# Kernel tuning notes

Hardware: AMD Instinct MI355X
Metric: run time of the kernel (lower is better)

Reference implementation:

```python
import jax, jax.numpy as jnp
import numpy as np

B, L, HID, D, H, HKV, EPS, THETA = 1, 2048, 2048, 128, 32, 4, 1e-6, 1000000.0
GROUPS = H // HKV  # 8


def setup_inputs() -> dict:
    key = jax.random.key(0)
    ks = jax.random.split(key, 6)
    x = jax.random.normal(ks[0], (B, L, HID), dtype=jnp.float32)
    wq = jax.random.normal(ks[1], (H * D, HID), dtype=jnp.float32) * 0.02
    wk = jax.random.normal(ks[2], (HKV * D, HID), dtype=jnp.float32) * 0.02
    wv = jax.random.normal(ks[3], (HKV * D, HID), dtype=jnp.float32) * 0.02
    wo = jax.random.normal(ks[4], (HID, H * D), dtype=jnp.float32) * 0.02
    q_norm_w = jnp.ones((D,), dtype=jnp.float32)
    k_norm_w = jnp.ones((D,), dtype=jnp.float32)
    # RoPE tables: inv_freq over half dims, emb = concat(freqs, freqs)
    inv_freq = 1.0 / (THETA ** (jnp.arange(0, D, 2, dtype=jnp.float32) / D))
    pos = jnp.arange(L, dtype=jnp.float32)
    freqs = pos[:, None] * inv_freq[None, :]        # [L, D/2]
    emb = jnp.concatenate([freqs, freqs], axis=-1)  # [L, D]
    cos = jnp.cos(emb)[None]                        # [1, L, D]
    sin = jnp.sin(emb)[None]
    return {"x": x, "wq": wq, "wk": wk, "wv": wv, "wo": wo,
            "q_norm_w": q_norm_w, "k_norm_w": k_norm_w, "cos": cos, "sin": sin}


def _rmsnorm(t, w):
    var = jnp.mean(t * t, axis=-1, keepdims=True)
    return t * jax.lax.rsqrt(var + EPS) * w


def _rotate_half(t):
    t1, t2 = jnp.split(t, 2, axis=-1)
    return jnp.concatenate([-t2, t1], axis=-1)


def reference(x, wq, wk, wv, wo, q_norm_w, k_norm_w, cos, sin):
    b, l, _ = x.shape
    # projections -> [B, heads, L, D]
    q = _rmsnorm((x @ wq.T).reshape(b, l, H, D), q_norm_w).swapaxes(1, 2)
    k = _rmsnorm((x @ wk.T).reshape(b, l, HKV, D), k_norm_w).swapaxes(1, 2)
    v = (x @ wv.T).reshape(b, l, HKV, D).swapaxes(1, 2)
    # RoPE (cos/sin broadcast over head dim)
    c, s = cos[:, None], sin[:, None]
    q = c * q + s * _rotate_half(q)
    k = c * k + s * _rotate_half(k)
    # GQA: repeat kv heads across groups
    k = jnp.repeat(k, GROUPS, axis=1)
    v = jnp.repeat(v, GROUPS, axis=1)
    # causal SDPA
    scores = jnp.einsum("bhqd,bhkd->bhqk", q, k) / np.sqrt(D).astype(np.float32)
    causal = jnp.tril(jnp.ones((l, l), dtype=bool))
    scores = jnp.where(causal, scores, jnp.finfo(scores.dtype).min)
    attn = jax.nn.softmax(scores, axis=-1)
    out = jnp.einsum("bhqk,bhkd->bhqd", attn, v)
    out = out.swapaxes(1, 2).reshape(b, l, H * D)
    return out @ wo.T
```

## Files before the change

### kernel.cpp

```cpp
#include <hip/hip_runtime.h>

typedef unsigned short u16;
typedef short bh8 __attribute__((ext_vector_type(8)));
typedef short bh4 __attribute__((ext_vector_type(4)));
typedef float f4 __attribute__((ext_vector_type(4)));
typedef u16 u16x4 __attribute__((ext_vector_type(4)));

__device__ __forceinline__ u16 f2bf(float f) {
  union { float f; unsigned u; } v; v.f = f;
  unsigned u = v.u;
  return (u16)((u + 0x7fffu + ((u >> 16) & 1u)) >> 16);
}
__device__ __forceinline__ float bf2f(u16 h) {
  union { unsigned u; float f; } v; v.u = ((unsigned)h) << 16;
  return v.f;
}
__device__ __forceinline__ float fast_exp2(float x) {
#if __has_builtin(__builtin_amdgcn_exp2f)
  return __builtin_amdgcn_exp2f(x);
#else
  float r; asm("v_exp_f32 %0, %1" : "=v"(r) : "v"(x)); return r;
#endif
}
__device__ __forceinline__ unsigned cvt_pk_bf16(float lo, float hi) {
  unsigned r;
  asm("v_cvt_pk_bf16_f32 %0, %1, %2" : "=v"(r) : "v"(lo), "v"(hi));
  return r;
}
__device__ __forceinline__ void gll16(const void* src, void* dst) {
  __builtin_amdgcn_global_load_lds((const __attribute__((address_space(1))) void*)src,
                                   (__attribute__((address_space(3))) void*)dst,
                                   16, 0, 0);
}

__global__ __launch_bounds__(256) void k_cvt_all(const float* __restrict__ x,
                                                 const float* __restrict__ wq,
                                                 const float* __restrict__ wk,
                                                 const float* __restrict__ wv,
                                                 const float* __restrict__ wo,
                                                 u16* __restrict__ dst) {
  const size_t n = 5767168;
  for (size_t idx = (size_t)blockIdx.x * 256 + threadIdx.x; idx < n; idx += 4096ull * 256) {
    const float* src; size_t off;
    if (idx < 1048576)       { src = x;  off = idx; }
    else if (idx < 3145728)  { src = wq; off = idx - 1048576; }
    else if (idx < 3407872)  { src = wk; off = idx - 3145728; }
    else if (idx < 3670016)  { src = wv; off = idx - 3407872; }
    else                     { src = wo; off = idx - 3670016; }
    f4 v = *(const f4*)(src + off * 4);
    u16x4 o;
    o.x = f2bf(v[0]); o.y = f2bf(v[1]); o.z = f2bf(v[2]); o.w = f2bf(v[3]);
    *(u16x4*)(dst + idx * 4) = o;
  }
}

template<int K, bool OUTF32, int NFR, bool FUSED>
__global__ __launch_bounds__(256) void k_gemm(const u16* __restrict__ A,
                                              const u16* __restrict__ B1,
                                              const u16* __restrict__ B2,
                                              void* __restrict__ C1,
                                              void* __restrict__ C2,
                                              int N1, int N2, int NB1, int npx) {
  constexpr int BN = NFR * 32;
  constexpr int nk = K / 32;
  __shared__ u16 As[3][128 * 32];
  __shared__ u16 Bs[3][BN * 32];
  const int t = threadIdx.x;
  const int lane = t & 63;
  const int w = t >> 6, wm = w >> 1, wn = w & 1;
  const int g = lane >> 4, r16 = lane & 15;
  const int bb = blockIdx.x;
  const int gl = (bb & 7) * npx + (bb >> 3);
  const int bm = gl & 15;
  int bn = gl >> 4;

  const u16* B; void* C; int N;
  if (!FUSED || bn < NB1) { B = B1; C = C1; N = N1; }
  else { bn -= NB1; B = B2; C = C2; N = N2; }
  B += (size_t)bn * BN * K;

  f4 acc[4][NFR] = {};

  const int rA0 = t >> 2, cA0 = (t & 3) * 8;
  const u16* a0 = A + (size_t)(bm * 128 + rA0) * K + cA0;
  const u16* a1 = a0 + (size_t)64 * K;
  const u16* b0 = B + (size_t)rA0 * K + cA0;

  auto STAGE = [&](int kk, int bi) {
    gll16(a0 + kk * 32, As[bi] + t * 8);
    gll16(a1 + kk * 32, As[bi] + (t + 256) * 8);
    gll16(b0 + kk * 32, Bs[bi] + t * 8);
    if constexpr (BN == 128) gll16(b0 + (size_t)64 * K + kk * 32, Bs[bi] + (t + 256) * 8);
  };
  auto COMP = [&](int bi) {
    bh8 af[4], bfr[NFR];
#pragma unroll
    for (int m = 0; m < 4; ++m)
      af[m] = *(const bh8*)&As[bi][(wm * 64 + m * 16 + r16) * 32 + g * 8];
#pragma unroll
    for (int n = 0; n < NFR; ++n)
      bfr[n] = *(const bh8*)&Bs[bi][(wn * 16 * NFR + n * 16 + r16) * 32 + g * 8];
    __builtin_amdgcn_s_setprio(1);
#pragma unroll
    for (int m = 0; m < 4; ++m)
#pragma unroll
      for (int n = 0; n < NFR; ++n)
        acc[m][n] = __builtin_amdgcn_mfma_f32_16x16x32_bf16(af[m], bfr[n], acc[m][n], 0, 0, 0);
    __builtin_amdgcn_s_setprio(0);
  };

  STAGE(0, 0);
  STAGE(1, 1);

  int bi = 0;
  for (int k = 0; k < nk - 2; ++k) {
    int st = bi + 2; if (st >= 3) st -= 3;
    STAGE(k + 2, st);
    if constexpr (BN == 128) asm volatile("s_waitcnt vmcnt(8)" ::: "memory");
    else                     asm volatile("s_waitcnt vmcnt(6)" ::: "memory");
    __builtin_amdgcn_s_barrier();
    __builtin_amdgcn_sched_barrier(0);
    COMP(bi);
    asm volatile("s_waitcnt lgkmcnt(0)" ::: "memory");
    __builtin_amdgcn_s_barrier();
    bi = (bi + 1 == 3) ? 0 : bi + 1;
  }
  if constexpr (BN == 128) asm volatile("s_waitcnt vmcnt(4)" ::: "memory");
  else                     asm volatile("s_waitcnt vmcnt(3)" ::: "memory");
  __builtin_amdgcn_s_barrier();
  __builtin_amdgcn_sched_barrier(0);
  COMP(bi);
  asm volatile("s_waitcnt lgkmcnt(0)" ::: "memory");
  __builtin_amdgcn_s_barrier();
  bi = (bi + 1 == 3) ? 0 : bi + 1;
  asm volatile("s_waitcnt vmcnt(0)" ::: "memory");
  __builtin_amdgcn_s_barrier();
  __builtin_amdgcn_sched_barrier(0);
  COMP(bi);

#pragma unroll
  for (int m = 0; m < 4; ++m) {
    const int row0 = bm * 128 + wm * 64 + m * 16 + g * 4;
#pragma unroll
    for (int n = 0; n < NFR; ++n) {
      const int col = bn * BN + wn * 16 * NFR + n * 16 + r16;
#pragma unroll
      for (int r = 0; r < 4; ++r) {
        if constexpr (OUTF32)
          ((float*)C)[(size_t)(row0 + r) * N + col] = acc[m][n][r];
        else
          ((u16*)C)[(size_t)(row0 + r) * N + col] = f2bf(acc[m][n][r]);
      }
    }
  }
}

__global__ __launch_bounds__(256) void k_normrope(u16* __restrict__ qbuf,
                                                  u16* __restrict__ kvbuf,
                                                  const float* __restrict__ qw,
                                                  const float* __restrict__ kw,
                                                  const float* __restrict__ cosb,
                                                  const float* __restrict__ sinb) {
  const float CSC = 1.4426950408889634f * 0.088388347648318447f;
  const int t = threadIdx.x, lane = t & 63, w = t >> 6;
  const int rid = blockIdx.x * 4 + w;
  u16* base; const float* nw; int seq; float sc;
  if (rid < 2048 * 32) {
    seq = rid >> 5;
    base = qbuf + (size_t)seq * 4096 + (size_t)(rid & 31) * 128;
    nw = qw; sc = CSC;
  } else {
    const int r2 = rid - 2048 * 32;
    seq = r2 >> 2;
    base = kvbuf + (size_t)seq * 1024 + (size_t)(r2 & 3) * 128;
    nw = kw; sc = 1.0f;
  }
  float a = bf2f(base[lane]);
  float b = bf2f(base[lane + 64]);
  float ss = a * a + b * b;
#pragma unroll
  for (int off = 32; off >= 1; off >>= 1) ss += __shfl_xor(ss, off);
  const float rs = rsqrtf(ss * (1.0f / 128.0f) + 1e-6f);
  const float na = a * rs * nw[lane];
  const float nb = b * rs * nw[lane + 64];
  const float c1 = cosb[seq * 128 + lane],      s1 = sinb[seq * 128 + lane];
  const float c2 = cosb[seq * 128 + lane + 64], s2 = sinb[seq * 128 + lane + 64];
  base[lane]      = f2bf(sc * (c1 * na - s1 * nb));
  base[lane + 64] = f2bf(sc * (c2 * nb + s2 * na));
}

__global__ __launch_bounds__(256) void k_transpose_v(const u16* __restrict__ kv,
                                                     u16* __restrict__ vt) {
  __shared__ u16 tile[32][33];
  const int t = threadIdx.x;
  const int bl = blockIdx.x, bh = blockIdx.y;
  const int row = t >> 3, c4 = (t & 7) * 4;
  const u16* src = kv + (size_t)(bl * 32 + row) * 1024 + 512 + bh * 32 + c4;
  u16x4 v = *(const u16x4*)src;
  tile[row][c4 + 0] = v.x; tile[row][c4 + 1] = v.y;
  tile[row][c4 + 2] = v.z; tile[row][c4 + 3] = v.w;
  __syncthreads();
  u16x4 o;
  o.x = tile[c4 + 0][row]; o.y = tile[c4 + 1][row];
  o.z = tile[c4 + 2][row]; o.w = tile[c4 + 3][row];
  const int pcol = ((c4 >> 2) & 3) * 8 + (c4 >> 4) * 4;
  *(u16x4*)&vt[(size_t)(bh * 32 + row) * 2048 + bl * 32 + pcol] = o;
}

__global__ __launch_bounds__(256, 3) void k_attn(const u16* __restrict__ Q,
                                                 const u16* __restrict__ Kb,
                                                 const u16* __restrict__ Vt,
                                                 u16* __restrict__ O) {
  __shared__ u16 Ks[2][64 * 128];
  __shared__ u16 Vs[128 * 64];
  const int t = threadIdx.x, lane = t & 63, w = t >> 6;
  const int g = lane >> 4, r16 = lane & 15;
  const int b = blockIdx.x;
  const int i = b & 31;
  const int qt = 31 - (b >> 5);
  const int h = ((i >> 1) & 3) * 8 + ((i & 1) << 2) + (i >> 3);
  const int kvh = h >> 3;
  const int qw0 = qt * 64 + w * 16;
  const int qg  = qw0 + r16;

  bh8 qf[4];
#pragma unroll
  for (int kc = 0; kc < 4; ++kc)
    qf[kc] = *(const bh8*)(Q + (size_t)qg * 4096 + h * 128 + (kc * 4 + g) * 8);

  const int niter = qt + 1;

  f4 acc_o[8] = {};
  f4 acc_l = {};
  float mrun = -3.0e38f;

  bh8 ones;
#pragma unroll
  for (int z = 0; z < 8; ++z) ones[z] = (short)0x3F80;

#pragma unroll
  for (int i2 = 0; i2 < 4; ++i2) {
    const int s = t + 256 * i2, row = s >> 4, sl = s & 15;
    gll16(Kb + (size_t)row * 1024 + kvh * 128 + ((sl ^ (row & 15)) * 8), Ks[0] + s * 8);
  }
  __syncthreads();

  int cur = 0;
  for (int kt = 0; kt < niter; ++kt) {
#pragma unroll
    for (int i2 = 0; i2 < 4; ++i2) {
      const int s = t + 256 * i2, row = s >> 3, sl = s & 7;
      gll16(Vt + (size_t)(kvh * 128 + row) * 2048 + kt * 64 + ((sl ^ (row & 7)) * 8),
            Vs + s * 8);
    }
    if (kt + 1 < niter) {
      const int nt = kt + 1;
#pragma unroll
      for (int i2 = 0; i2 < 4; ++i2) {
        const int s = t + 256 * i2, row = s >> 4, sl = s & 15;
        gll16(Kb + (size_t)(nt * 64 + row) * 1024 + kvh * 128 + ((sl ^ (row & 15)) * 8),
              Ks[cur ^ 1] + s * 8);
      }
    }

    f4 st[4] = {};
    __builtin_amdgcn_s_setprio(1);
#pragma unroll
    for (int kf = 0; kf < 4; ++kf) {
      const int krow = kf * 16 + r16;
#pragma unroll
      for (int kc = 0; kc < 4; ++kc) {
        bh8 kfr = *(const bh8*)&Ks[cur][krow * 128 + (((kc * 4 + g) ^ (krow & 15)) * 8)];
        st[kf] = __builtin_amdgcn_mfma_f32_16x16x32_bf16(kfr, qf[kc], st[kf], 0, 0, 0);
      }
    }
    __builtin_amdgcn_s_setprio(0);

    if (kt == qt) {
      const int kb = kt * 64 + g * 4;
#pragma unroll
      for (int kf = 0; kf < 4; ++kf)
#pragma unroll
        for (int r = 0; r < 4; ++r)
          if (kb + kf * 16 + r > qg) st[kf][r] = -3.0e38f;
    }

    f4 m4;
#pragma unroll
    for (int r = 0; r < 4; ++r)
      m4[r] = fmaxf(fmaxf(st[0][r], st[1][r]), fmaxf(st[2][r], st[3][r]));
    float tmax = fmaxf(fmaxf(m4[0], m4[1]), fmaxf(m4[2], m4[3]));
    tmax = fmaxf(tmax, __shfl_xor(tmax, 16));
    tmax = fmaxf(tmax, __shfl_xor(tmax, 32));

    if (!__all(tmax <= mrun + 8.0f)) {
      const float mnew = fmaxf(mrun, tmax);
      const float alpha = fast_exp2(mrun - mnew);
      mrun = mnew;
      acc_l *= alpha;
#pragma unroll
      for (int d = 0; d < 8; ++d) acc_o[d] *= alpha;
    }

    union { bh8 v[2]; unsigned wrd[8]; } pu;
#pragma unroll
    for (int j = 0; j < 8; ++j) {
      const int i0 = 2 * j, i1 = 2 * j + 1;
      float p0 = fast_exp2(st[i0 >> 2][i0 & 3] - mrun);
      float p1 = fast_exp2(st[i1 >> 2][i1 & 3] - mrun);
      pu.wrd[j] = cvt_pk_bf16(p0, p1);
    }

    __syncthreads();

    __builtin_amdgcn_s_setprio(1);
#pragma unroll
    for (int c = 0; c < 2; ++c)
      acc_l = __builtin_amdgcn_mfma_f32_16x16x32_bf16(ones, pu.v[c], acc_l, 0, 0, 0);
#pragma unroll
    for (int dcol = 0; dcol < 8; ++dcol) {
      const int vrow = dcol * 16 + r16;
#pragma unroll
      for (int c = 0; c < 2; ++c) {
        const int slot = c * 4 + g;
        bh8 vfr = *(const bh8*)&Vs[vrow * 64 + ((slot ^ (vrow & 7)) * 8)];
        acc_o[dcol] = __builtin_amdgcn_mfma_f32_16x16x32_bf16(vfr, pu.v[c], acc_o[dcol], 0, 0, 0);
      }
    }
    __builtin_amdgcn_s_setprio(0);

    __syncthreads();
    cur ^= 1;
  }

  const float inv = 1.0f / acc_l[0];
#pragma unroll
  for (int dcol = 0; dcol < 8; ++dcol) {
    union { u16x4 v; unsigned wrd[2]; } o;
    o.wrd[0] = cvt_pk_bf16(acc_o[dcol][0] * inv, acc_o[dcol][1] * inv);
    o.wrd[1] = cvt_pk_bf16(acc_o[dcol][2] * inv, acc_o[dcol][3] * inv);
    *(u16x4*)&O[(size_t)qg * 4096 + h * 128 + dcol * 16 + g * 4] = o.v;
  }
}

extern "C" void kernel_launch(void* const* d_in, const int* in_sizes, int n_in,
                              void* d_out, int out_size, void* d_ws, size_t ws_size,
                              hipStream_t stream) {
  (void)in_sizes; (void)n_in; (void)out_size; (void)ws_size;
  const float* x    = (const float*)d_in[0];
  const float* wq   = (const float*)d_in[1];
  const float* wk   = (const float*)d_in[2];
  const float* wv   = (const float*)d_in[3];
  const float* wo   = (const float*)d_in[4];
  const float* qw   = (const float*)d_in[5];
  const float* kw   = (const float*)d_in[6];
  const float* cosb = (const float*)d_in[7];
  const float* sinb = (const float*)d_in[8];

  u16* xb   = (u16*)d_ws;
  u16* wqb  = xb  + (size_t)2048 * 2048;
  u16* wkvb = wqb + (size_t)4096 * 2048;
  u16* wob  = wkvb + (size_t)1024 * 2048;
  u16* qbuf = wob + (size_t)2048 * 4096;
  u16* kvb  = qbuf + (size_t)2048 * 4096;
  u16* vt   = kvb + (size_t)2048 * 1024;
  u16* aout = vt  + (size_t)512 * 2048;

  k_cvt_all<<<dim3(4096), 256, 0, stream>>>(x, wq, wk, wv, wo, xb);

  k_gemm<2048, false, 4, true><<<dim3(640), 256, 0, stream>>>(
      xb, wqb, wkvb, qbuf, kvb, 4096, 1024, 32, 80);

  k_normrope<<<dim3((2048 * 36) / 4), 256, 0, stream>>>(qbuf, kvb, qw, kw, cosb, sinb);

  k_transpose_v<<<dim3(64, 16), 256, 0, stream>>>(kvb, vt);

  k_attn<<<dim3(1024), 256, 0, stream>>>(qbuf, kvb, vt, aout);

  k_gemm<4096, true, 2, false><<<dim3(512), 256, 0, stream>>>(
      aout, wob, nullptr, d_out, nullptr, 2048, 0, 0, 64);
}
```

Baseline: 208.3 us.

## Fuse V transpose into QKV GEMM epilogue and deepen K tile for output GEMM

The QKV GEMM now writes V blocks directly in the transposed, permuted layout the attention kernel expects, so the separate transpose kernel and its launch are removed. The shared-memory layout becomes k-group-major so tiles can be staged with a parameterised BK. The output projection GEMM uses BK=64, which halves its k-iterations and barriers but doubles its LDS footprint. This risks layout mismatches in the fused V writes and lower occupancy in the output GEMM.

```diff
diff --git a/kernel.cpp b/kernel.cpp
--- a/kernel.cpp
+++ b/kernel.cpp
@@ -54,17 +54,24 @@
   }
 }
 
-template<int K, bool OUTF32, int NFR, bool FUSED>
+template<int K, bool OUTF32, int NFR, bool FUSED, int BK>
 __global__ __launch_bounds__(256) void k_gemm(const u16* __restrict__ A,
                                               const u16* __restrict__ B1,
                                               const u16* __restrict__ B2,
                                               void* __restrict__ C1,
                                               void* __restrict__ C2,
+                                              u16* __restrict__ Cv,
                                               int N1, int N2, int NB1, int npx) {
   constexpr int BN = NFR * 32;
-  constexpr int nk = K / 32;
-  __shared__ u16 As[3][128 * 32];
-  __shared__ u16 Bs[3][BN * 32];
+  constexpr int nk = K / BK;
+  constexpr int ASZ = 128 * BK;
+  constexpr int BSZ = BN * BK;
+  constexpr int LA = ASZ / 2048;
+  constexpr int LB = BSZ / 2048;
+  constexpr int LPS = LA + LB;
+  constexpr int LOGBN = (BN == 128) ? 7 : 6;
+  __shared__ u16 As[3][ASZ];
+  __shared__ u16 Bs[3][BSZ];
   const int t = threadIdx.x;
   const int lane = t & 63;
   const int w = t >> 6, wm = w >> 1, wn = w & 1;
@@ -74,39 +81,47 @@
   const int bm = gl & 15;
   int bn = gl >> 4;
 
-  const u16* B; void* C; int N;
+  const u16* B; void* C; int N; bool vpath = false;
   if (!FUSED || bn < NB1) { B = B1; C = C1; N = N1; }
-  else { bn -= NB1; B = B2; C = C2; N = N2; }
+  else { bn -= NB1; B = B2; C = C2; N = N2; vpath = (bn >= 4); }
   B += (size_t)bn * BN * K;
+  const u16* Ab = A + (size_t)bm * 128 * K;
 
   f4 acc[4][NFR] = {};
 
-  const int rA0 = t >> 2, cA0 = (t & 3) * 8;
-  const u16* a0 = A + (size_t)(bm * 128 + rA0) * K + cA0;
-  const u16* a1 = a0 + (size_t)64 * K;
-  const u16* b0 = B + (size_t)rA0 * K + cA0;
-
   auto STAGE = [&](int kk, int bi) {
-    gll16(a0 + kk * 32, As[bi] + t * 8);
-    gll16(a1 + kk * 32, As[bi] + (t + 256) * 8);
-    gll16(b0 + kk * 32, Bs[bi] + t * 8);
-    if constexpr (BN == 128) gll16(b0 + (size_t)64 * K + kk * 32, Bs[bi] + (t + 256) * 8);
+    const int k0 = kk * BK;
+#pragma unroll
+    for (int i2 = 0; i2 < LA; ++i2) {
+      const int s = t + 256 * i2;
+      const int g2 = s >> 7, row = s & 127;
+      gll16(Ab + (size_t)row * K + k0 + g2 * 8, As[bi] + s * 8);
+    }
+#pragma unroll
+    for (int i2 = 0; i2 < LB; ++i2) {
+      const int s = t + 256 * i2;
+      const int g2 = s >> LOGBN, col = s & (BN - 1);
+      gll16(B + (size_t)col * K + k0 + g2 * 8, Bs[bi] + s * 8);
+    }
   };
   auto COMP = [&](int bi) {
-    bh8 af[4], bfr[NFR];
-#pragma unroll
-    for (int m = 0; m < 4; ++m)
-      af[m] = *(const bh8*)&As[bi][(wm * 64 + m * 16 + r16) * 32 + g * 8];
-#pragma unroll
-    for (int n = 0; n < NFR; ++n)
-      bfr[n] = *(const bh8*)&Bs[bi][(wn * 16 * NFR + n * 16 + r16) * 32 + g * 8];
-    __builtin_amdgcn_s_setprio(1);
-#pragma unroll
-    for (int m = 0; m < 4; ++m)
+#pragma unroll
+    for (int kk = 0; kk < BK / 32; ++kk) {
+      bh8 af[4], bfr[NFR];
+#pragma unroll
+      for (int m = 0; m < 4; ++m)
+        af[m] = *(const bh8*)&As[bi][((kk * 4 + g) * 128 + (wm * 64 + m * 16 + r16)) * 8];
 #pragma unroll
       for (int n = 0; n < NFR; ++n)
-        acc[m][n] = __builtin_amdgcn_mfma_f32_16x16x32_bf16(af[m], bfr[n], acc[m][n], 0, 0, 0);
-    __builtin_amdgcn_s_setprio(0);
+        bfr[n] = *(const bh8*)&Bs[bi][((kk * 4 + g) * BN + (wn * 16 * NFR + n * 16 + r16)) * 8];
+      __builtin_amdgcn_s_setprio(1);
+#pragma unroll
+      for (int m = 0; m < 4; ++m)
+#pragma unroll
+        for (int n = 0; n < NFR; ++n)
+          acc[m][n] = __builtin_amdgcn_mfma_f32_16x16x32_bf16(af[m], bfr[n], acc[m][n], 0, 0, 0);
+      __builtin_amdgcn_s_setprio(0);
+    }
   };
 
   STAGE(0, 0);
@@ -116,8 +131,8 @@
   for (int k = 0; k < nk - 2; ++k) {
     int st = bi + 2; if (st >= 3) st -= 3;
     STAGE(k + 2, st);
-    if constexpr (BN == 128) asm volatile("s_waitcnt vmcnt(8)" ::: "memory");
-    else                     asm volatile("s_waitcnt vmcnt(6)" ::: "memory");
+    if constexpr (LPS == 4) asm volatile("s_waitcnt vmcnt(8)" ::: "memory");
+    else                    asm volatile("s_waitcnt vmcnt(12)" ::: "memory");
     __builtin_amdgcn_s_barrier();
     __builtin_amdgcn_sched_barrier(0);
     COMP(bi);
@@ -125,8 +140,8 @@
     __builtin_amdgcn_s_barrier();
     bi = (bi + 1 == 3) ? 0 : bi + 1;
   }
-  if constexpr (BN == 128) asm volatile("s_waitcnt vmcnt(4)" ::: "memory");
-  else                     asm volatile("s_waitcnt vmcnt(3)" ::: "memory");
+  if constexpr (LPS == 4) asm volatile("s_waitcnt vmcnt(4)" ::: "memory");
+  else                    asm volatile("s_waitcnt vmcnt(6)" ::: "memory");
   __builtin_amdgcn_s_barrier();
   __builtin_amdgcn_sched_barrier(0);
   COMP(bi);
@@ -137,6 +152,24 @@
   __builtin_amdgcn_s_barrier();
   __builtin_amdgcn_sched_barrier(0);
   COMP(bi);
+
+  if constexpr (FUSED) {
+    if (vpath) {
+#pragma unroll
+      for (int m = 0; m < 4; ++m) {
+        const int lp = bm * 128 + wm * 64 + (m >> 1) * 32 + g * 8 + (m & 1) * 4;
+#pragma unroll
+        for (int n = 0; n < NFR; ++n) {
+          const int col = bn * BN + wn * 16 * NFR + n * 16 + r16;
+          union { u16x4 v; unsigned wrd[2]; } o;
+          o.wrd[0] = cvt_pk_bf16(acc[m][n][0], acc[m][n][1]);
+          o.wrd[1] = cvt_pk_bf16(acc[m][n][2], acc[m][n][3]);
+          *(u16x4*)&Cv[(size_t)(col - 512) * 2048 + lp] = o.v;
+        }
+      }
+      return;
+    }
+  }
 
 #pragma unroll
   for (int m = 0; m < 4; ++m) {
@@ -189,24 +222,6 @@
   base[lane + 64] = f2bf(sc * (c2 * nb + s2 * na));
 }
 
-__global__ __launch_bounds__(256) void k_transpose_v(const u16* __restrict__ kv,
-                                                     u16* __restrict__ vt) {
-  __shared__ u16 tile[32][33];
-  const int t = threadIdx.x;
-  const int bl = blockIdx.x, bh = blockIdx.y;
-  const int row = t >> 3, c4 = (t & 7) * 4;
-  const u16* src = kv + (size_t)(bl * 32 + row) * 1024 + 512 + bh * 32 + c4;
-  u16x4 v = *(const u16x4*)src;
-  tile[row][c4 + 0] = v.x; tile[row][c4 + 1] = v.y;
-  tile[row][c4 + 2] = v.z; tile[row][c4 + 3] = v.w;
-  __syncthreads();
-  u16x4 o;
-  o.x = tile[c4 + 0][row]; o.y = tile[c4 + 1][row];
-  o.z = tile[c4 + 2][row]; o.w = tile[c4 + 3][row];
-  const int pcol = ((c4 >> 2) & 3) * 8 + (c4 >> 4) * 4;
-  *(u16x4*)&vt[(size_t)(bh * 32 + row) * 2048 + bl * 32 + pcol] = o;
-}
-
 __global__ __launch_bounds__(256, 3) void k_attn(const u16* __restrict__ Q,
                                                  const u16* __restrict__ Kb,
                                                  const u16* __restrict__ Vt,
@@ -368,15 +383,13 @@
 
   k_cvt_all<<<dim3(4096), 256, 0, stream>>>(x, wq, wk, wv, wo, xb);
 
-  k_gemm<2048, false, 4, true><<<dim3(640), 256, 0, stream>>>(
-      xb, wqb, wkvb, qbuf, kvb, 4096, 1024, 32, 80);
+  k_gemm<2048, false, 4, true, 32><<<dim3(640), 256, 0, stream>>>(
+      xb, wqb, wkvb, qbuf, kvb, vt, 4096, 1024, 32, 80);
 
   k_normrope<<<dim3((2048 * 36) / 4), 256, 0, stream>>>(qbuf, kvb, qw, kw, cosb, sinb);
 
-  k_transpose_v<<<dim3(64, 16), 256, 0, stream>>>(kvb, vt);
-
   k_attn<<<dim3(1024), 256, 0, stream>>>(qbuf, kvb, vt, aout);
 
-  k_gemm<4096, true, 2, false><<<dim3(512), 256, 0, stream>>>(
-      aout, wob, nullptr, d_out, nullptr, 2048, 0, 0, 64);
-}
+  k_gemm<4096, true, 2, false, 64><<<dim3(512), 256, 0, stream>>>(
+      aout, wob, nullptr, d_out, nullptr, nullptr, 2048, 0, 0, 64);
+}
```

After: 285.3 us. +37.0%, slower.
